# Optimization experiments

Hardware: AMD Instinct MI355X
Metric: run time of the kernel (lower is better)

Reference implementation:

```python
import jax, jax.numpy as jnp
import numpy as np

N = 50000   # nodes
E = 800000  # edges
F = 128     # num_node_features
H = 256     # hidden_channels
C = 40      # num_classes


def setup_inputs() -> dict:
    key = jax.random.key(0)
    ks = jax.random.split(key, 8)
    x = jax.random.normal(ks[0], (N, F), dtype=jnp.float32)
    edge_index = jax.random.randint(ks[1], (2, E), 0, N, dtype=jnp.int32)
    # GCNConv linear weights (PyG: lin has no bias; bias added post-aggregation)
    W1 = jax.random.normal(ks[2], (H, F), dtype=jnp.float32) * (1.0 / np.sqrt(F))
    b1 = jnp.zeros((H,), dtype=jnp.float32)
    W2 = jax.random.normal(ks[3], (H, H), dtype=jnp.float32) * (1.0 / np.sqrt(H))
    b2 = jnp.zeros((H,), dtype=jnp.float32)
    Wout = jax.random.normal(ks[4], (C, H), dtype=jnp.float32) * (1.0 / np.sqrt(H))
    bout = jnp.zeros((C,), dtype=jnp.float32)
    return {"x": x, "edge_index": edge_index,
            "W1": W1, "b1": b1, "W2": W2, "b2": b2,
            "Wout": Wout, "bout": bout}


def gcn_conv(x, src, dst, W, b, n):
    """PyG GCNConv: sym-normalized aggregation with self-loops.
    deg computed as in-degree on dst (gcn_norm), +1 for self loop.
    """
    h = x @ W.T  # [n, out]
    ones = jnp.ones((src.shape[0],), dtype=h.dtype)
    deg = jax.ops.segment_sum(ones, dst, num_segments=n) + 1.0  # self loop
    dinv = jax.lax.rsqrt(deg)  # deg >= 1, safe
    norm = dinv[src] * dinv[dst]                 # [E]
    agg = jax.ops.segment_sum(norm[:, None] * h[src], dst, num_segments=n)
    agg = agg + (dinv * dinv)[:, None] * h       # self-loop term
    return agg + b


def reference(x, edge_index, W1, b1, W2, b2, Wout, bout):
    src, dst = edge_index[0], edge_index[1]
    h = jax.nn.relu(gcn_conv(x, src, dst, W1, b1, N))
    h = gcn_conv(h, src, dst, W2, b2, N)
    return h @ Wout.T + bout  # [N, C] logits
```

## Files before the change

kernel.cpp:

```cpp
#include <hip/hip_runtime.h>

#define N_NODES 50000
#define N_EDGES 800000
#define F_IN    128
#define H_DIM   256
#define C_OUT   40
#define MT_TOT  (N_NODES / 16)
#define NBIN1   196
#define CAP     5120
#define NCHB    200
#define CHSZ    (N_EDGES / NCHB)
#define CVT_X   (N_NODES * F_IN / 4)
#define XVB     ((CVT_X + 255) / 256)
#define CVT_W1B (H_DIM * F_IN / 4 / 256)

typedef unsigned short u16;
typedef unsigned int   u32;
typedef short bf16x8 __attribute__((ext_vector_type(8)));
typedef float f32x4  __attribute__((ext_vector_type(4)));

__device__ inline float bfbits2f(u16 u) { return __uint_as_float(((u32)u) << 16); }
__device__ inline u16 f2bf(float f) {
    u32 u = __float_as_uint(f);
    u += 0x7fffu + ((u >> 16) & 1u);
    return (u16)(u >> 16);
}
__device__ inline u32 pack2(float a, float b) {
    return (u32)f2bf(a) | ((u32)f2bf(b) << 16);
}

__global__ __launch_bounds__(256) void mega1_k(const int* __restrict__ src, const int* __restrict__ dst,
                                               int* __restrict__ bincnt, uint2* __restrict__ T,
                                               const float4* __restrict__ x, uint2* __restrict__ xb,
                                               const float4* __restrict__ W1, uint2* __restrict__ W1b,
                                               const float* __restrict__ W2, const float* __restrict__ Wo,
                                               const float* __restrict__ b2, const float* __restrict__ bo,
                                               u16* __restrict__ Wcb, float* __restrict__ bc) {
    __shared__ int hist[NBIN1];
    __shared__ int curp[NBIN1];
    __shared__ float red[256];
    const int t = threadIdx.x;
    if (blockIdx.x < NCHB) {
        const int b = blockIdx.x;
        if (t < NBIN1) hist[t] = 0;
        __syncthreads();
        for (int i = b * CHSZ + t; i < (b + 1) * CHSZ; i += 256)
            atomicAdd(&hist[dst[i] >> 8], 1);
        __syncthreads();
        if (t < NBIN1) curp[t] = atomicAdd(&bincnt[t], hist[t]);
        __syncthreads();
        for (int i = b * CHSZ + t; i < (b + 1) * CHSZ; i += 256) {
            const int s = src[i], d = dst[i];
            const int bin = d >> 8;
            const int idx = atomicAdd(&curp[bin], 1);
            uint2 ed; ed.x = (u32)s; ed.y = (u32)d;
            T[(size_t)bin * CAP + idx] = ed;
        }
        return;
    }
    if (blockIdx.x < NCHB + XVB) {
        const int i = (blockIdx.x - NCHB) * 256 + t;
        if (i >= CVT_X) return;
        float4 v = x[i];
        uint2 o; o.x = pack2(v.x, v.y); o.y = pack2(v.z, v.w);
        xb[i] = o;
        return;
    }
    if (blockIdx.x < NCHB + XVB + CVT_W1B) {
        int i = (blockIdx.x - NCHB - XVB) * 256 + t;
        float4 v = W1[i];
        uint2 o; o.x = pack2(v.x, v.y); o.y = pack2(v.z, v.w);
        W1b[i] = o;
        return;
    }
    const int c = blockIdx.x - NCHB - XVB - CVT_W1B;
    float acc = 0.f;
    for (int o = 0; o < H_DIM; o += 8) {
        float w2v[8];
#pragma unroll
        for (int j = 0; j < 8; j++) w2v[j] = W2[(size_t)(o + j) * H_DIM + t];
#pragma unroll
        for (int j = 0; j < 8; j++) acc += Wo[(size_t)c * H_DIM + o + j] * w2v[j];
    }
    Wcb[(size_t)c * H_DIM + t] = f2bf(acc);
    red[t] = b2[t] * Wo[(size_t)c * H_DIM + t];
    __syncthreads();
    for (int off = 128; off > 0; off >>= 1) {
        if (t < off) red[t] += red[t + off];
        __syncthreads();
    }
    if (t == 0) bc[c] = red[0] + bo[c];
}

__global__ __launch_bounds__(256) void p3_k(const uint2* __restrict__ T, const int* __restrict__ bincnt,
                                            u32* __restrict__ rowinfo, float* __restrict__ dinv,
                                            u32* __restrict__ edata) {
    __shared__ int hcnt[256];
    __shared__ int sc[256];
    __shared__ int cur[256];
    const int t = threadIdx.x;
    const int g = blockIdx.x;
    const int nbeg = g * CAP;
    const int nend = nbeg + bincnt[g];
    hcnt[t] = 0;
    __syncthreads();
    for (int i = nbeg + t; i < nend; i += 256)
        atomicAdd(&hcnt[T[i].y & 255], 1);
    __syncthreads();
    const int my = hcnt[t];
    sc[t] = my;
    __syncthreads();
    for (int off = 1; off < 256; off <<= 1) {
        int u = (t >= off) ? sc[t - off] : 0;
        __syncthreads();
        sc[t] += u;
        __syncthreads();
    }
    const int rbeg = nbeg + sc[t] - my;
    const int node = g * 256 + t;
    if (node < N_NODES) {
        rowinfo[node] = ((u32)my << 20) | (u32)rbeg;
        dinv[node] = rsqrtf((float)my + 1.0f);
    }
    cur[t] = rbeg;
    __syncthreads();
    for (int i = nbeg + t; i < nend; i += 256) {
        const uint2 e = T[i];
        const int pos = atomicAdd(&cur[e.y & 255], 1);
        edata[pos] = e.x;
    }
}

__global__ __launch_bounds__(256) void gather1_k(const u32* __restrict__ xb,
                                                 const u32* __restrict__ rowinfo,
                                                 const u32* __restrict__ edata,
                                                 const float* __restrict__ dinv,
                                                 u32* __restrict__ aggx) {
    const int node = __builtin_amdgcn_readfirstlane(blockIdx.x * 4 + (threadIdx.x >> 6));
    const int lane = threadIdx.x & 63;
    if (node >= N_NODES) return;
    const u32 info = __builtin_amdgcn_readfirstlane(rowinfo[node]);
    const int beg = (int)(info & 0xFFFFFu);
    const int end = beg + (int)(info >> 20);
    const float dd = dinv[node];
    const u32 vs = xb[(size_t)node * 64 + lane];
    float a0 = dd * bfbits2f((u16)vs);
    float a1 = dd * bfbits2f((u16)(vs >> 16));
    int e = beg;
    for (; e + 7 < end; e += 8) {
        u32 s8[8];
#pragma unroll
        for (int j = 0; j < 8; j++) s8[j] = edata[e + j];
        float dv8[8];
#pragma unroll
        for (int j = 0; j < 8; j++) dv8[j] = dinv[s8[j]];
        u32 v[8];
#pragma unroll
        for (int j = 0; j < 8; j++) v[j] = xb[(size_t)s8[j] * 64 + lane];
#pragma unroll
        for (int j = 0; j < 8; j++) {
            a0 += dv8[j] * bfbits2f((u16)v[j]);
            a1 += dv8[j] * bfbits2f((u16)(v[j] >> 16));
        }
    }
    for (; e < end; e++) {
        const u32 s = edata[e];
        const float dv = dinv[s];
        const u32 v0 = xb[(size_t)s * 64 + lane];
        a0 += dv * bfbits2f((u16)v0);
        a1 += dv * bfbits2f((u16)(v0 >> 16));
    }
    aggx[(size_t)node * 64 + lane] = pack2(dd * a0, dd * a1);
}

__global__ __launch_bounds__(256) void bgemm1f_k(const u16* __restrict__ X,
                                                 const u16* __restrict__ W1b,
                                                 const float* __restrict__ b1,
                                                 const u16* __restrict__ Wcb,
                                                 const float* __restrict__ dinv,
                                                 u16* __restrict__ tb) {
    constexpr int KF1 = F_IN / 32;
    constexpr int KF2 = H_DIM / 32;
    __shared__ __align__(16) u16 hs[2][16][H_DIM + 8];
    const int wave = threadIdx.x >> 6;
    const int lane = threadIdx.x & 63;
    const int quad = lane >> 4;
    const int nn = lane & 15;
    const int ngbase = wave * 64;

    bf16x8 Bf[4][KF1];
    float bb[4];
#pragma unroll
    for (int j = 0; j < 4; j++) {
        const int wr = ngbase + j * 16 + nn;
#pragma unroll
        for (int kf = 0; kf < KF1; kf++)
            Bf[j][kf] = *(const bf16x8*)(W1b + (size_t)wr * F_IN + kf * 32 + quad * 8);
        bb[j] = b1[wr];
    }
    bf16x8 Bh[KF2];
    {
        int hr = wave * 16 + nn;
        if (hr > C_OUT - 1) hr = C_OUT - 1;
#pragma unroll
        for (int kf = 0; kf < KF2; kf++)
            Bh[kf] = *(const bf16x8*)(Wcb + (size_t)hr * H_DIM + kf * 32 + quad * 8);
    }

    int mt = blockIdx.x;
    if (mt >= MT_TOT) return;
    const int stride = gridDim.x;
    int buf = 0;

    bf16x8 Acur[KF1], Anext[KF1];
    {
        const u16* ap = X + (size_t)(mt * 16 + nn) * F_IN + quad * 8;
#pragma unroll
        for (int kf = 0; kf < KF1; kf++) Acur[kf] = *(const bf16x8*)(ap + kf * 32);
    }

    while (true) {
        const int mtn = mt + stride;
        if (mtn < MT_TOT) {
            const u16* ap = X + (size_t)(mtn * 16 + nn) * F_IN + quad * 8;
#pragma unroll
            for (int kf = 0; kf < KF1; kf++) Anext[kf] = *(const bf16x8*)(ap + kf * 32);
        }

        f32x4 acc[4];
#pragma unroll
        for (int j = 0; j < 4; j++) acc[j] = (f32x4){0.f, 0.f, 0.f, 0.f};
#pragma unroll
        for (int kf = 0; kf < KF1; kf++)
#pragma unroll
            for (int j = 0; j < 4; j++)
                acc[j] = __builtin_amdgcn_mfma_f32_16x16x32_bf16(Acur[kf], Bf[j][kf], acc[j], 0, 0, 0);

#pragma unroll
        for (int j = 0; j < 4; j++)
#pragma unroll
            for (int r = 0; r < 4; r++)
                hs[buf][quad * 4 + r][ngbase + j * 16 + nn] = f2bf(fmaxf(acc[j][r] + bb[j], 0.f));
        __syncthreads();

        if (wave < 3) {
            f32x4 ah = (f32x4){0.f, 0.f, 0.f, 0.f};
#pragma unroll
            for (int kf = 0; kf < KF2; kf++) {
                bf16x8 af = *(const bf16x8*)(&hs[buf][nn][kf * 32 + quad * 8]);
                ah = __builtin_amdgcn_mfma_f32_16x16x32_bf16(af, Bh[kf], ah, 0, 0, 0);
            }
            const int col = wave * 16 + nn;
            if (col < C_OUT) {
#pragma unroll
                for (int r = 0; r < 4; r++) {
                    const int row = mt * 16 + quad * 4 + r;
                    tb[(size_t)row * C_OUT + col] = f2bf(dinv[row] * ah[r]);
                }
            }
        }

        if (mtn >= MT_TOT) break;
#pragma unroll
        for (int kf = 0; kf < KF1; kf++) Acur[kf] = Anext[kf];
        mt = mtn;
        buf ^= 1;
    }
}

__global__ __launch_bounds__(256) void gatherO_k(const u32* __restrict__ tb,
                                                 const u32* __restrict__ rowinfo,
                                                 const u32* __restrict__ edata,
                                                 const float* __restrict__ dinv,
                                                 const float* __restrict__ bc,
                                                 float* __restrict__ out) {
    const int node = __builtin_amdgcn_readfirstlane(blockIdx.x * 4 + (threadIdx.x >> 6));
    const int lane = threadIdx.x & 63;
    if (node >= N_NODES) return;
    const int lc = lane & 31;
    const bool act = (lc < C_OUT / 2);
    const u32 info = __builtin_amdgcn_readfirstlane(rowinfo[node]);
    const int beg = (int)(info & 0xFFFFFu);
    const int end = beg + (int)(info >> 20);
    const float dd = dinv[node];
    const u32 vs = act ? tb[(size_t)node * (C_OUT / 2) + lc] : 0u;
    float a0 = bfbits2f((u16)vs);
    float a1 = bfbits2f((u16)(vs >> 16));
    int e = beg;
    for (; e + 7 < end; e += 8) {
        u32 s8[8];
#pragma unroll
        for (int j = 0; j < 8; j++) s8[j] = edata[e + j];
        u32 v[8];
#pragma unroll
        for (int j = 0; j < 8; j++) v[j] = act ? tb[(size_t)s8[j] * (C_OUT / 2) + lc] : 0u;
#pragma unroll
        for (int j = 0; j < 8; j++) {
            a0 += bfbits2f((u16)v[j]);
            a1 += bfbits2f((u16)(v[j] >> 16));
        }
    }
    for (; e < end; e++) {
        const u32 v0 = act ? tb[(size_t)edata[e] * (C_OUT / 2) + lc] : 0u;
        a0 += bfbits2f((u16)v0);
        a1 += bfbits2f((u16)(v0 >> 16));
    }
    if (lane < C_OUT / 2) {
        float2 o;
        o.x = dd * a0 + bc[2 * lane];
        o.y = dd * a1 + bc[2 * lane + 1];
        *(float2*)(out + (size_t)node * C_OUT + 2 * lane) = o;
    }
}

extern "C" void kernel_launch(void* const* d_in, const int* in_sizes, int n_in,
                              void* d_out, int out_size, void* d_ws, size_t ws_size,
                              hipStream_t stream) {
    const float* x    = (const float*)d_in[0];
    const int*   ei   = (const int*)d_in[1];
    const float* W1   = (const float*)d_in[2];
    const float* b1   = (const float*)d_in[3];
    const float* W2   = (const float*)d_in[4];
    const float* b2   = (const float*)d_in[5];
    const float* Wout = (const float*)d_in[6];
    const float* bout = (const float*)d_in[7];
    float* out = (float*)d_out;

    const int* src = ei;
    const int* dst = ei + N_EDGES;

    char* ws = (char*)d_ws;
    size_t o = 0;
    auto alloc = [&](size_t bytes) { size_t p = o; o = (o + bytes + 255) & ~(size_t)255; return p; };
    int*   bincnt = (int*)(ws + alloc((size_t)NBIN1 * 4));
    float* dinv   = (float*)(ws + alloc((size_t)N_NODES * 4));
    u32*   rowinfo= (u32*)(ws + alloc((size_t)N_NODES * 4));
    uint2* T      = (uint2*)(ws + alloc((size_t)NBIN1 * CAP * 8));
    u32*   edata  = (u32*)(ws + alloc((size_t)NBIN1 * CAP * 4));
    u16*   xb     = (u16*)(ws + alloc((size_t)N_NODES * F_IN * 2));
    u16*   aggxb  = (u16*)(ws + alloc((size_t)N_NODES * F_IN * 2));
    u16*   tb     = (u16*)(ws + alloc((size_t)N_NODES * C_OUT * 2 + 256));
    u16*   W1b    = (u16*)(ws + alloc((size_t)H_DIM * F_IN * 2));
    u16*   Wcb    = (u16*)(ws + alloc((size_t)C_OUT * H_DIM * 2));
    float* bc     = (float*)(ws + alloc((size_t)C_OUT * 4));

    hipMemsetAsync(bincnt, 0, (size_t)NBIN1 * 4, stream);
    mega1_k<<<NCHB + XVB + CVT_W1B + C_OUT, 256, 0, stream>>>(
        src, dst, bincnt, T, (const float4*)x, (uint2*)xb,
        (const float4*)W1, (uint2*)W1b, W2, Wout, b2, bout, Wcb, bc);
    p3_k<<<NBIN1, 256, 0, stream>>>(T, bincnt, rowinfo, dinv, edata);

    gather1_k<<<(N_NODES + 3) / 4, 256, 0, stream>>>((const u32*)xb, rowinfo, edata, dinv, (u32*)aggxb);
    bgemm1f_k<<<768, 256, 0, stream>>>(aggxb, W1b, b1, Wcb, dinv, tb);
    gatherO_k<<<(N_NODES + 3) / 4, 256, 0, stream>>>((const u32*)tb, rowinfo, edata, dinv, bc, out);
}
```

Before: 188.9 us.

## Fuse CSR build phase into mega kernel with global done-counter spin wait

Merges the p3 bin-sort kernel into the first mega kernel. Its 196 blocks spin on a global atomic counter until all histogram/scatter blocks finish, which removes one kernel launch and lets the conversion blocks overlap with the sort. The number of scatter chunks is doubled to 400 for more parallelism, and the output-store predicate in gatherO is changed to use act/lc. The spin-wait could deadlock if the waiting blocks occupy all CUs before the producer blocks are scheduled, but blocks are ordered so producers get lower IDs.

Result: slower. 287.4 us (+52.1%).

```diff
diff --git a/kernel.cpp b/kernel.cpp
--- a/kernel.cpp
+++ b/kernel.cpp
@@ -8,7 +8,7 @@
 #define MT_TOT  (N_NODES / 16)
 #define NBIN1   196
 #define CAP     5120
-#define NCHB    200
+#define NCHB    400
 #define CHSZ    (N_EDGES / NCHB)
 #define CVT_X   (N_NODES * F_IN / 4)
 #define XVB     ((CVT_X + 255) / 256)
@@ -29,15 +29,21 @@
     return (u32)f2bf(a) | ((u32)f2bf(b) << 16);
 }
 
-__global__ __launch_bounds__(256) void mega1_k(const int* __restrict__ src, const int* __restrict__ dst,
-                                               int* __restrict__ bincnt, uint2* __restrict__ T,
-                                               const float4* __restrict__ x, uint2* __restrict__ xb,
-                                               const float4* __restrict__ W1, uint2* __restrict__ W1b,
-                                               const float* __restrict__ W2, const float* __restrict__ Wo,
-                                               const float* __restrict__ b2, const float* __restrict__ bo,
-                                               u16* __restrict__ Wcb, float* __restrict__ bc) {
+__global__ __launch_bounds__(256) void mega_k(const int* __restrict__ src, const int* __restrict__ dst,
+                                              int* __restrict__ bincnt, int* __restrict__ done,
+                                              uint2* __restrict__ T,
+                                              u32* __restrict__ rowinfo, float* __restrict__ dinv,
+                                              u32* __restrict__ edata,
+                                              const float4* __restrict__ x, uint2* __restrict__ xb,
+                                              const float4* __restrict__ W1, uint2* __restrict__ W1b,
+                                              const float* __restrict__ W2, const float* __restrict__ Wo,
+                                              const float* __restrict__ b2, const float* __restrict__ bo,
+                                              u16* __restrict__ Wcb, float* __restrict__ bc) {
     __shared__ int hist[NBIN1];
     __shared__ int curp[NBIN1];
+    __shared__ int hcnt[256];
+    __shared__ int sc[256];
+    __shared__ int cur[256];
     __shared__ float red[256];
     const int t = threadIdx.x;
     if (blockIdx.x < NCHB) {
@@ -56,24 +62,67 @@
             uint2 ed; ed.x = (u32)s; ed.y = (u32)d;
             T[(size_t)bin * CAP + idx] = ed;
         }
+        __syncthreads();
+        if (t == 0) {
+            __threadfence();
+            __hip_atomic_fetch_add(done, 1, __ATOMIC_RELEASE, __HIP_MEMORY_SCOPE_AGENT);
+        }
         return;
     }
-    if (blockIdx.x < NCHB + XVB) {
-        const int i = (blockIdx.x - NCHB) * 256 + t;
+    if (blockIdx.x < NCHB + NBIN1) {
+        if (t == 0) {
+            while (__hip_atomic_load(done, __ATOMIC_ACQUIRE, __HIP_MEMORY_SCOPE_AGENT) != NCHB)
+                __builtin_amdgcn_s_sleep(8);
+        }
+        __syncthreads();
+        const int g = blockIdx.x - NCHB;
+        const int nbeg = g * CAP;
+        const int nend = nbeg + bincnt[g];
+        hcnt[t] = 0;
+        __syncthreads();
+        for (int i = nbeg + t; i < nend; i += 256)
+            atomicAdd(&hcnt[T[i].y & 255], 1);
+        __syncthreads();
+        const int my = hcnt[t];
+        sc[t] = my;
+        __syncthreads();
+        for (int off = 1; off < 256; off <<= 1) {
+            int u = (t >= off) ? sc[t - off] : 0;
+            __syncthreads();
+            sc[t] += u;
+            __syncthreads();
+        }
+        const int rbeg = nbeg + sc[t] - my;
+        const int node = g * 256 + t;
+        if (node < N_NODES) {
+            rowinfo[node] = ((u32)my << 20) | (u32)rbeg;
+            dinv[node] = rsqrtf((float)my + 1.0f);
+        }
+        cur[t] = rbeg;
+        __syncthreads();
+        for (int i = nbeg + t; i < nend; i += 256) {
+            const uint2 e = T[i];
+            const int pos = atomicAdd(&cur[e.y & 255], 1);
+            edata[pos] = e.x;
+        }
+        return;
+    }
+    if (blockIdx.x < NCHB + NBIN1 + XVB) {
+        const int i = (blockIdx.x - NCHB - NBIN1) * 256 + t;
         if (i >= CVT_X) return;
         float4 v = x[i];
         uint2 o; o.x = pack2(v.x, v.y); o.y = pack2(v.z, v.w);
         xb[i] = o;
         return;
     }
-    if (blockIdx.x < NCHB + XVB + CVT_W1B) {
-        int i = (blockIdx.x - NCHB - XVB) * 256 + t;
+    if (blockIdx.x < NCHB + NBIN1 + XVB + CVT_W1B) {
+        int i = (blockIdx.x - NCHB - NBIN1 - XVB) * 256 + t;
         float4 v = W1[i];
         uint2 o; o.x = pack2(v.x, v.y); o.y = pack2(v.z, v.w);
         W1b[i] = o;
         return;
     }
-    const int c = blockIdx.x - NCHB - XVB - CVT_W1B;
+    const int c = blockIdx.x - NCHB - NBIN1 - XVB - CVT_W1B;
     float acc = 0.f;
     for (int o = 0; o < H_DIM; o += 8) {
         float w2v[8];
@@ -90,45 +139,6 @@
         __syncthreads();
     }
     if (t == 0) bc[c] = red[0] + bo[c];
-}
-
-__global__ __launch_bounds__(256) void p3_k(const uint2* __restrict__ T, const int* __restrict__ bincnt,
-                                            u32* __restrict__ rowinfo, float* __restrict__ dinv,
-                                            u32* __restrict__ edata) {
-    __shared__ int hcnt[256];
-    __shared__ int sc[256];
-    __shared__ int cur[256];
-    const int t = threadIdx.x;
-    const int g = blockIdx.x;
-    const int nbeg = g * CAP;
-    const int nend = nbeg + bincnt[g];
-    hcnt[t] = 0;
-    __syncthreads();
-    for (int i = nbeg + t; i < nend; i += 256)
-        atomicAdd(&hcnt[T[i].y & 255], 1);
-    __syncthreads();
-    const int my = hcnt[t];
-    sc[t] = my;
-    __syncthreads();
-    for (int off = 1; off < 256; off <<= 1) {
-        int u = (t >= off) ? sc[t - off] : 0;
-        __syncthreads();
-        sc[t] += u;
-        __syncthreads();
-    }
-    const int rbeg = nbeg + sc[t] - my;
-    const int node = g * 256 + t;
-    if (node < N_NODES) {
-        rowinfo[node] = ((u32)my << 20) | (u32)rbeg;
-        dinv[node] = rsqrtf((float)my + 1.0f);
-    }
-    cur[t] = rbeg;
-    __syncthreads();
-    for (int i = nbeg + t; i < nend; i += 256) {
-        const uint2 e = T[i];
-        const int pos = atomicAdd(&cur[e.y & 255], 1);
-        edata[pos] = e.x;
-    }
 }
 
 __global__ __launch_bounds__(256) void gather1_k(const u32* __restrict__ xb,
@@ -305,11 +315,11 @@
         a0 += bfbits2f((u16)v0);
         a1 += bfbits2f((u16)(v0 >> 16));
     }
-    if (lane < C_OUT / 2) {
+    if (act) {
         float2 o;
-        o.x = dd * a0 + bc[2 * lane];
-        o.y = dd * a1 + bc[2 * lane + 1];
-        *(float2*)(out + (size_t)node * C_OUT + 2 * lane) = o;
+        o.x = dd * a0 + bc[2 * lc];
+        o.y = dd * a1 + bc[2 * lc + 1];
+        *(float2*)(out + (size_t)node * C_OUT + 2 * lc) = o;
     }
 }
 
@@ -332,7 +342,8 @@
     char* ws = (char*)d_ws;
     size_t o = 0;
     auto alloc = [&](size_t bytes) { size_t p = o; o = (o + bytes + 255) & ~(size_t)255; return p; };
-    int*   bincnt = (int*)(ws + alloc((size_t)NBIN1 * 4));
+    int*   bincnt = (int*)(ws + alloc((size_t)(NBIN1 + 1) * 4));
+    int*   done   = bincnt + NBIN1;
     float* dinv   = (float*)(ws + alloc((size_t)N_NODES * 4));
     u32*   rowinfo= (u32*)(ws + alloc((size_t)N_NODES * 4));
     uint2* T      = (uint2*)(ws + alloc((size_t)NBIN1 * CAP * 8));
@@ -344,11 +355,11 @@
     u16*   Wcb    = (u16*)(ws + alloc((size_t)C_OUT * H_DIM * 2));
     float* bc     = (float*)(ws + alloc((size_t)C_OUT * 4));
 
-    hipMemsetAsync(bincnt, 0, (size_t)NBIN1 * 4, stream);
-    mega1_k<<<NCHB + XVB + CVT_W1B + C_OUT, 256, 0, stream>>>(
-        src, dst, bincnt, T, (const float4*)x, (uint2*)xb,
+    hipMemsetAsync(bincnt, 0, (size_t)(NBIN1 + 1) * 4, stream);
+    mega_k<<<NCHB + NBIN1 + XVB + CVT_W1B + C_OUT, 256, 0, stream>>>(
+        src, dst, bincnt, done, T, rowinfo, dinv, edata,
+        (const float4*)x, (uint2*)xb,
         (const float4*)W1, (uint2*)W1b, W2, Wout, b2, bout, Wcb, bc);
-    p3_k<<<NBIN1, 256, 0, stream>>>(T, bincnt, rowinfo, dinv, edata);
 
     gather1_k<<<(N_NODES + 3) / 4, 256, 0, stream>>>((const u32*)xb, rowinfo, edata, dinv, (u32*)aggxb);
     bgemm1f_k<<<768, 256, 0, stream>>>(aggxb, W1b, b1, Wcb, dinv, tb);
```
